# Kernel optimization log

Measured on AMD Instinct MI355X. Metric: run time of the kernel, lower is better.

## Reference

```python
import jax, jax.numpy as jnp
import numpy as np

SLOPE = 0.2  # LeakyReLU slope (DGCNN convention)

def _conv1x1(x, W, b):
    # x: [B, N, Cin], W: [Cout, Cin] -> [B, N, Cout] (Conv2d 1x1 == shared MLP)
    return jnp.einsum('bnc,oc->bno', x, W) + b

def _edgeconv(x, k, Wa, ba, Wb, bb):
    # DGCNN EdgeConv: kNN in feature space, edge MLP on (x_j - x_i, x_i), max-aggregate.
    # x: [B, N, C]
    sq = jnp.sum(x * x, axis=-1)                       # [B, N]
    inner = jnp.einsum('bnc,bmc->bnm', x, x)           # [B, N, N]
    dist = sq[:, :, None] - 2.0 * inner + sq[:, None, :]
    _, idx = jax.lax.top_k(-dist, k)                   # [B, N, k] (includes self)
    nb = jax.vmap(lambda xb, ib: xb[ib])(x, idx)       # [B, N, k, C] gather neighbors
    xi = jnp.broadcast_to(x[:, :, None, :], nb.shape)
    e = jnp.concatenate([nb - xi, xi], axis=-1)        # [B, N, k, 2C]
    h = jax.nn.leaky_relu(jnp.einsum('bnke,oe->bnko', e, Wa) + ba, SLOPE)
    h = jax.nn.leaky_relu(jnp.einsum('bnkc,oc->bnko', h, Wb) + bb, SLOPE)
    return jnp.max(h, axis=2)                          # [B, N, Cout]

def setup_inputs() -> dict:
    key = jax.random.key(0)
    ks = jax.random.split(key, 12)
    B, C, N = 2, 128, 8192
    r = 4
    out_dim = 3 * r  # 12
    def w(k, shape, fan_in):
        return (jax.random.normal(k, shape, jnp.float32) / np.sqrt(fan_in)).astype(jnp.float32)
    z = lambda n: jnp.zeros((n,), jnp.float32)
    return {
        'feature': jax.random.normal(ks[0], (B, C, N, 1), jnp.float32),
        # block 0: conv_bn_layer 128->32, EdgeConv(32->128, k=12)
        'Wc0': w(ks[1], (32, 128), 128), 'bc0': z(32),
        'We0a': w(ks[2], (128, 64), 64), 'be0a': z(128),
        'We0b': w(ks[3], (128, 128), 128), 'be0b': z(128),
        # block 1: conv_bn_layer 128->32, EdgeConv(32->128, k=4)
        'Wc1': w(ks[4], (32, 128), 128), 'bc1': z(32),
        'We1a': w(ks[5], (128, 64), 64), 'be1a': z(128),
        'We1b': w(ks[6], (128, 128), 128), 'be1b': z(128),
        # decoder: shared MLP [128 -> 6 -> 12], then Conv2d(12, 12, 1) with bias
        'Wd0': w(ks[7], (out_dim // 2, 128), 128), 'bd0': z(out_dim // 2),
        'Wd1': w(ks[8], (out_dim, out_dim // 2), out_dim // 2), 'bd1': z(out_dim),
        'Wd2': w(ks[9], (out_dim, out_dim), out_dim), 'bd2': z(out_dim),
    }

def reference(feature, Wc0, bc0, We0a, be0a, We0b, be0b,
              Wc1, bc1, We1a, be1a, We1b, be1b,
              Wd0, bd0, Wd1, bd1, Wd2, bd2):
    # feature: [B, C, N, 1] -> [B, N, C]
    x = jnp.swapaxes(jnp.squeeze(feature, -1), 1, 2)
    x = jax.nn.leaky_relu(_conv1x1(x, Wc0, bc0), SLOPE)   # 128 -> 32
    x = _edgeconv(x, 12, We0a, be0a, We0b, be0b)           # 32 -> 128, k=12
    x = jax.nn.leaky_relu(_conv1x1(x, Wc1, bc1), SLOPE)   # 128 -> 32
    x = _edgeconv(x, 4, We1a, be1a, We1b, be1b)            # 32 -> 128, k=4
    x = jax.nn.leaky_relu(_conv1x1(x, Wd0, bd0), SLOPE)   # 128 -> 6
    x = jax.nn.leaky_relu(_conv1x1(x, Wd1, bd1), SLOPE)   # 6 -> 12
    x = _conv1x1(x, Wd2, bd2)                              # final conv, no activation
    return x  # [B, N, 3*upsample_ratio] (matches squeeze(-1).permute(0,2,1))
```

## Files before the change

### kernel.cpp

```cpp
#include <hip/hip_runtime.h>

#define NPTS 8192
#define NB 2

typedef __attribute__((ext_vector_type(8))) short short8v;
typedef __attribute__((ext_vector_type(4))) float f32x4;

__device__ __forceinline__ float lrelu(float x) { return x > 0.f ? x : 0.2f * x; }
__device__ __forceinline__ float4 lrelu4(float4 a) {
    return make_float4(lrelu(a.x), lrelu(a.y), lrelu(a.z), lrelu(a.w));
}
__device__ __forceinline__ float4 fmax4(float4 a, float4 b) {
    return make_float4(fmaxf(a.x, b.x), fmaxf(a.y, b.y), fmaxf(a.z, b.z), fmaxf(a.w, b.w));
}
__device__ __forceinline__ float4 add4(float4 a, float4 b) {
    return make_float4(a.x + b.x, a.y + b.y, a.z + b.z, a.w + b.w);
}
__device__ __forceinline__ unsigned short f2bf(float f) {
    unsigned int u = __float_as_uint(f);
    return (unsigned short)((u + 0x7FFFu + ((u >> 16) & 1u)) >> 16);
}
__device__ __forceinline__ float bf2f(unsigned short h) {
    return __uint_as_float(((unsigned int)h) << 16);
}

__global__ void k_transpose_w(const float* __restrict__ Wb0, const float* __restrict__ Wb1,
                              float* __restrict__ out) {
    int t = blockIdx.x * 256 + threadIdx.x;
    if (t < 16384)      out[t] = Wb0[(t & 127) * 128 + (t >> 7)];
    else if (t < 32768) { int i = t - 16384; out[t] = Wb1[(i & 127) * 128 + (i >> 7)]; }
}

__device__ __forceinline__ void split3(float4 v, unsigned int* hp, unsigned int* mp,
                                       unsigned int* lp) {
    float c[4] = {v.x, v.y, v.z, v.w};
    unsigned short h[4], m[4], l[4];
    #pragma unroll
    for (int i = 0; i < 4; ++i) {
        h[i] = f2bf(c[i]);
        float r1 = c[i] - bf2f(h[i]);
        m[i] = f2bf(r1);
        float r2 = r1 - bf2f(m[i]);
        l[i] = f2bf(r2);
    }
    hp[0] = (unsigned int)h[0] | ((unsigned int)h[1] << 16);
    hp[1] = (unsigned int)h[2] | ((unsigned int)h[3] << 16);
    mp[0] = (unsigned int)m[0] | ((unsigned int)m[1] << 16);
    mp[1] = (unsigned int)m[2] | ((unsigned int)m[3] << 16);
    lp[0] = (unsigned int)l[0] | ((unsigned int)l[1] << 16);
    lp[1] = (unsigned int)l[2] | ((unsigned int)l[3] << 16);
}

__global__ void k_conv_in(const float* __restrict__ f, const float* __restrict__ W,
                          const float* __restrict__ bias, float* __restrict__ out,
                          float* __restrict__ sq, unsigned short* __restrict__ xh,
                          unsigned short* __restrict__ xm, unsigned short* __restrict__ xl) {
    int gid = blockIdx.x * blockDim.x + threadIdx.x;
    int b = gid >> 13, n = gid & (NPTS - 1);
    const float* fb = f + ((size_t)b << 20) + n;
    float acc[32];
    #pragma unroll
    for (int o = 0; o < 32; ++o) acc[o] = bias[o];
    #pragma unroll 4
    for (int c = 0; c < 128; ++c) {
        float xc = fb[(size_t)c * NPTS];
        #pragma unroll
        for (int o = 0; o < 32; ++o) acc[o] += xc * W[o * 128 + c];
    }
    float s = 0.f;
    float4* op = (float4*)(out + (size_t)gid * 32);
    unsigned int* hrow = (unsigned int*)(xh + (size_t)gid * 32);
    unsigned int* mrow = (unsigned int*)(xm + (size_t)gid * 32);
    unsigned int* lrow = (unsigned int*)(xl + (size_t)gid * 32);
    #pragma unroll
    for (int o4 = 0; o4 < 8; ++o4) {
        float4 v = make_float4(lrelu(acc[o4 * 4]), lrelu(acc[o4 * 4 + 1]),
                               lrelu(acc[o4 * 4 + 2]), lrelu(acc[o4 * 4 + 3]));
        s += v.x * v.x + v.y * v.y + v.z * v.z + v.w * v.w;
        op[o4] = v;
        unsigned int hp[2], mp[2], lp[2];
        split3(v, hp, mp, lp);
        *(uint2*)(hrow + o4 * 2) = make_uint2(hp[0], hp[1]);
        *(uint2*)(mrow + o4 * 2) = make_uint2(mp[0], mp[1]);
        *(uint2*)(lrow + o4 * 2) = make_uint2(lp[0], lp[1]);
    }
    sq[gid] = s;
}

__global__ __launch_bounds__(256, 2) void k_premix(const float* __restrict__ x,
                                                   const float* __restrict__ Wa,
                                                   const float* __restrict__ ba,
                                                   float* __restrict__ A,
                                                   float* __restrict__ Bm) {
    int tid = threadIdx.x;
    int q = tid >> 6;
    int p = blockIdx.x * 64 + (tid & 63);
    float4 xv[8];
    {
        const float4* xr = (const float4*)(x + (size_t)p * 32);
        #pragma unroll
        for (int u = 0; u < 8; ++u) xv[u] = xr[u];
    }
    const float* W0 = Wa + q * 32 * 64;
    float acc[32];
    #pragma unroll
    for (int o = 0; o < 32; ++o) acc[o] = 0.f;
    #pragma unroll 2
    for (int c4 = 0; c4 < 8; ++c4) {
        float4 v = xv[c4];
        #pragma unroll
        for (int o = 0; o < 32; ++o) {
            const float* w = W0 + o * 64 + c4 * 4;
            acc[o] += v.x * w[0] + v.y * w[1] + v.z * w[2] + v.w * w[3];
        }
    }
    {
        float4* op = (float4*)(A + (size_t)p * 128 + q * 32);
        #pragma unroll
        for (int o4 = 0; o4 < 8; ++o4)
            op[o4] = make_float4(acc[o4 * 4], acc[o4 * 4 + 1], acc[o4 * 4 + 2], acc[o4 * 4 + 3]);
    }
    #pragma unroll
    for (int o = 0; o < 32; ++o) acc[o] = ba[q * 32 + o];
    #pragma unroll 2
    for (int c4 = 0; c4 < 8; ++c4) {
        float4 v = xv[c4];
        #pragma unroll
        for (int o = 0; o < 32; ++o) {
            const float* w1 = W0 + o * 64 + c4 * 4;
            const float* w2 = w1 + 32;
            acc[o] += v.x * (w2[0] - w1[0]) + v.y * (w2[1] - w1[1]) +
                      v.z * (w2[2] - w1[2]) + v.w * (w2[3] - w1[3]);
        }
    }
    {
        float4* op = (float4*)(Bm + (size_t)p * 128 + q * 32);
        #pragma unroll
        for (int o4 = 0; o4 < 8; ++o4)
            op[o4] = make_float4(acc[o4 * 4], acc[o4 * 4 + 1], acc[o4 * 4 + 2], acc[o4 * 4 + 3]);
    }
}

template <int K, int JS, int C>
__global__ __launch_bounds__(128, 2) void k_knn_mfma(const unsigned short* __restrict__ xh,
                                                     const unsigned short* __restrict__ xm,
                                                     const unsigned short* __restrict__ xl,
                                                     const float* __restrict__ sqg,
                                                     float* __restrict__ cand_d,
                                                     int* __restrict__ cand_i) {
    constexpr int IT = 128;
    constexpr int JR = NPTS / JS;
    constexpr int NCH = JR / 16;
    constexpr int BPB = (NPTS / IT) * JS;
    constexpr int DS = 17;

    __shared__ float Dl[IT * DS];
    __shared__ float SQl[2][16];
    __shared__ float bufd[C * IT];
    __shared__ int   bufj[C * IT];

    int tid = threadIdx.x;
    int bid = blockIdx.x;
    int b = bid / BPB;
    int r0b = bid - b * BPB;
    int itile = r0b / JS;
    int jseg = r0b - itile * JS;

    const unsigned short* xhb = xh + ((size_t)b * NPTS) * 32;
    const unsigned short* xmb = xm + ((size_t)b * NPTS) * 32;
    const unsigned short* xlb = xl + ((size_t)b * NPTS) * 32;
    const float* sqb = sqg + (size_t)b * NPTS;

    int lane = tid & 63;
    int w = tid >> 6;
    int g = lane >> 4;
    int r15 = lane & 15;

    short8v ah[4], am[4], al[4];
    #pragma unroll
    for (int t = 0; t < 4; ++t) {
        size_t ii = (size_t)(itile * IT + w * 64 + t * 16 + r15);
        ah[t] = *(const short8v*)(xhb + ii * 32 + g * 8);
        am[t] = *(const short8v*)(xmb + ii * 32 + g * 8);
        al[t] = *(const short8v*)(xlb + ii * 32 + g * 8);
    }
    #pragma unroll
    for (int t = 0; t < 4; ++t) {
        asm volatile("" : "+v"(ah[t]));
        asm volatile("" : "+v"(am[t]));
        asm volatile("" : "+v"(al[t]));
    }

    float bd[K]; int bi[K];
    #pragma unroll
    for (int r = 0; r < K; ++r) { bd[r] = 1e30f; bi[r] = 0; }
    float thr = 1e30f;
    int cnt = 0;

    auto flush = [&]() {
        #pragma unroll
        for (int u = 0; u < C; ++u) {
            float dv = bufd[u * IT + tid];
            int jv = bufj[u * IT + tid];
            float dd = (u < cnt) ? dv : 1e30f;
            int ji = jv;
            #pragma unroll
            for (int r = 0; r < K; ++r) {
                bool c = dd < bd[r];
                float tf = bd[r]; int ti = bi[r];
                bd[r] = c ? dd : bd[r]; bi[r] = c ? ji : bi[r];
                dd = c ? tf : dd;       ji = c ? ti : ji;
            }
        }
        cnt = 0; thr = bd[K - 1];
    };

#define LOADB_(J, BH, BM, BL)                                                  \
    do {                                                                       \
        size_t ja_ = (size_t)(J) + r15;                                        \
        BH = *(const short8v*)(xhb + ja_ * 32 + g * 8);                        \
        BM = *(const short8v*)(xmb + ja_ * 32 + g * 8);                        \
        BL = *(const short8v*)(xlb + ja_ * 32 + g * 8);                        \
    } while (0)

#define SQSTAGE_(J0)                                                           \
    do {                                                                       \
        if (g == 0) SQl[w][r15] = sqb[(J0) + r15];                             \
    } while (0)

#define MFMA_(BH, BM, BL)                                                      \
    do {                                                                       \
        _Pragma("unroll")                                                      \
        for (int t = 0; t < 4; ++t) {                                          \
            f32x4 acc = {0.f, 0.f, 0.f, 0.f};                                  \
            acc = __builtin_amdgcn_mfma_f32_16x16x32_bf16(am[t], BM, acc, 0, 0, 0); \
            acc = __builtin_amdgcn_mfma_f32_16x16x32_bf16(ah[t], BL, acc, 0, 0, 0); \
            acc = __builtin_amdgcn_mfma_f32_16x16x32_bf16(al[t], BH, acc, 0, 0, 0); \
            acc = __builtin_amdgcn_mfma_f32_16x16x32_bf16(ah[t], BM, acc, 0, 0, 0); \
            acc = __builtin_amdgcn_mfma_f32_16x16x32_bf16(am[t], BH, acc, 0, 0, 0); \
            acc = __builtin_amdgcn_mfma_f32_16x16x32_bf16(ah[t], BH, acc, 0, 0, 0); \
            int il_ = w * 64 + t * 16 + g * 4;                                 \
            Dl[(il_ + 0) * DS + r15] = acc[0];                                 \
            Dl[(il_ + 1) * DS + r15] = acc[1];                                 \
            Dl[(il_ + 2) * DS + r15] = acc[2];                                 \
            Dl[(il_ + 3) * DS + r15] = acc[3];                                 \
        }                                                                      \
    } while (0)

#define SELECT_(J0)                                                            \
    do {                                                                       \
        _Pragma("unroll 1")                                                    \
        for (int jq = 0; jq < 16; jq += 4) {                                   \
            float v0 = Dl[tid * DS + jq + 0];                                  \
            float v1 = Dl[tid * DS + jq + 1];                                  \
            float v2 = Dl[tid * DS + jq + 2];                                  \
            float v3 = Dl[tid * DS + jq + 3];                                  \
            float s0 = SQl[w][jq + 0];                                         \
            float s1 = SQl[w][jq + 1];                                         \
            float s2 = SQl[w][jq + 2];                                         \
            float s3 = SQl[w][jq + 3];                                         \
            int j_ = (J0) + jq;                                                \
            float d0 = s0 - 2.f * v0;                                          \
            float d1 = s1 - 2.f * v1;                                          \
            float d2 = s2 - 2.f * v2;                                          \
            float d3 = s3 - 2.f * v3;                                          \
            if (d0 < thr) { bufd[cnt * IT + tid] = d0; bufj[cnt * IT + tid] = j_ + 0; cnt++; } \
            if (d1 < thr) { bufd[cnt * IT + tid] = d1; bufj[cnt * IT + tid] = j_ + 1; cnt++; } \
            if (d2 < thr) { bufd[cnt * IT + tid] = d2; bufj[cnt * IT + tid] = j_ + 2; cnt++; } \
            if (d3 < thr) { bufd[cnt * IT + tid] = d3; bufj[cnt * IT + tid] = j_ + 3; cnt++; } \
            if (__any(cnt >= C - 3)) flush();                                  \
        }                                                                      \
    } while (0)

    int jbase = jseg * JR;
    short8v bhA, bmA, blA, bhB, bmB, blB;
    LOADB_(jbase, bhA, bmA, blA);
    #pragma unroll 1
    for (int ch = 0; ch < NCH; ch += 2) {
        int j0 = jbase + ch * 16;
        int j1 = j0 + 16;
        SQSTAGE_(j0);
        LOADB_(j1, bhB, bmB, blB);
        MFMA_(bhA, bmA, blA);
        SELECT_(j0);
        SQSTAGE_(j1);
        int j2 = (ch + 2 < NCH) ? j1 + 16 : jbase;
        LOADB_(j2, bhA, bmA, blA);
        MFMA_(bhB, bmB, blB);
        SELECT_(j1);
    }
    flush();
#undef LOADB_
#undef SQSTAGE_
#undef MFMA_
#undef SELECT_
    size_t base = ((size_t)jseg * (NB * NPTS) + (size_t)(b * NPTS) + itile * IT + tid) * K;
    #pragma unroll
    for (int r = 0; r < K; ++r) { cand_d[base + r] = bd[r]; cand_i[base + r] = bi[r]; }
}

template <int K, int JS>
__global__ __launch_bounds__(128, 4) void k_knn_merge2(const float* __restrict__ cand_d,
                                                       const int* __restrict__ cand_i,
                                                       int* __restrict__ idx_out) {
    int p = blockIdx.x * 128 + threadIdx.x;
    float bd[K]; int bi[K];
    #pragma unroll
    for (int r = 0; r < K; ++r) { bd[r] = 1e30f; bi[r] = 0; }
    float thr = 1e30f;
    #pragma unroll 1
    for (int s = 0; s < JS; ++s) {
        size_t base = ((size_t)s * (NB * NPTS) + p) * K;
        #pragma unroll 1
        for (int r = 0; r < K; ++r) {
            float d = cand_d[base + r];
            if (!(d < thr)) break;
            int j = cand_i[base + r];
            float dd = d; int ji = j;
            #pragma unroll
            for (int q = 0; q < K; ++q) {
                bool c = dd < bd[q];
                float tf = bd[q]; int ti = bi[q];
                bd[q] = c ? dd : bd[q]; bi[q] = c ? ji : bi[q];
                dd = c ? tf : dd;       ji = c ? ti : ji;
            }
            thr = bd[K - 1];
        }
    }
    int* op = idx_out + (size_t)p * K;
    #pragma unroll
    for (int r = 0; r < K; ++r) op[r] = bi[r];
}

template <int K>
__global__ __launch_bounds__(256, 1)
void k_edgeconv4(const int* __restrict__ idx,
                 const float* __restrict__ A, const float* __restrict__ Bm,
                 const float* __restrict__ WbTg, const float* __restrict__ bb,
                 float* __restrict__ y) {
    constexpr int TE = (K == 12) ? 6 : 4;
    constexpr int EPI = 16 * TE;
    constexpr int PI = EPI / K;
    constexpr int ITERS = 64 / PI;
    constexpr int NT = 256;
    constexpr int HS = 132;

    __shared__ __align__(16) float WbT[128 * 128];
    __shared__ __align__(16) float bb_s[128];
    __shared__ __align__(16) float H1[EPI * HS];
    __shared__ __align__(16) float Pm[(K == 12) ? 16 * 128 : 4];

    int tid = threadIdx.x;
    {
        const float4* sb = (const float4*)WbTg;
        float4* db = (float4*)WbT;
        #pragma unroll
        for (int i = 0; i < 16; ++i) db[tid + i * NT] = sb[tid + i * NT];
        if (tid < 128) bb_s[tid] = bb[tid];
    }

    int b = blockIdx.x >> 7;
    int pbase = (blockIdx.x & 127) * 64;
    const int* idxb = idx + ((size_t)b * NPTS) * K;
    const float4* A4 = (const float4*)(A + ((size_t)b * NPTS) * 128);
    const float4* B4 = (const float4*)(Bm + ((size_t)b * NPTS) * 128);
    float* yb = y + ((size_t)b * NPTS) * 128;

    int og = tid & 15;
    int eg = tid >> 4;
    int ebase = eg * TE;

    for (int it = 0; it < ITERS; ++it) {
        int pt0 = pbase + it * PI;
        #pragma unroll
        for (int r = 0; r < (EPI * 32) / NT; ++r) {
            int u = tid + r * NT;
            int e = u >> 5, c4 = u & 31;
            int p = pt0 + e / K;
            int j = idxb[(size_t)p * K + (e % K)];
            float4 av = A4[(size_t)j * 32 + c4];
            float4 bv = B4[(size_t)p * 32 + c4];
            *(float4*)&H1[e * HS + 4 * c4] = lrelu4(add4(av, bv));
        }
        __syncthreads();
        float4 acc[TE][2];
        {
            float4 blo = *(const float4*)&bb_s[og * 8];
            float4 bhi = *(const float4*)&bb_s[og * 8 + 4];
            #pragma unroll
            for (int e = 0; e < TE; ++e) { acc[e][0] = blo; acc[e][1] = bhi; }
        }
        #pragma unroll 2
        for (int c4 = 0; c4 < 32; ++c4) {
            float4 hv[TE];
            #pragma unroll
            for (int e = 0; e < TE; ++e)
                hv[e] = *(const float4*)&H1[(ebase + e) * HS + 4 * c4];
            #pragma unroll
            for (int j = 0; j < 4; ++j) {
                const float* wr = &WbT[(4 * c4 + j) * 128 + og * 8];
                float4 wlo = *(const float4*)wr;
                float4 whi = *(const float4*)(wr + 4);
                #pragma unroll
                for (int e = 0; e < TE; ++e) {
                    float hc = (j == 0) ? hv[e].x : (j == 1) ? hv[e].y : (j == 2) ? hv[e].z : hv[e].w;
                    acc[e][0].x += hc * wlo.x; acc[e][0].y += hc * wlo.y;
                    acc[e][0].z += hc * wlo.z; acc[e][0].w += hc * wlo.w;
                    acc[e][1].x += hc * whi.x; acc[e][1].y += hc * whi.y;
                    acc[e][1].z += hc * whi.z; acc[e][1].w += hc * whi.w;
                }
            }
        }
        float4 mlo = lrelu4(acc[0][0]), mhi = lrelu4(acc[0][1]);
        #pragma unroll
        for (int e = 1; e < TE; ++e) {
            mlo = fmax4(mlo, lrelu4(acc[e][0]));
            mhi = fmax4(mhi, lrelu4(acc[e][1]));
        }
        if constexpr (K == 4) {
            float4* yp = (float4*)&yb[((size_t)(pt0 + eg)) * 128 + og * 8];
            yp[0] = mlo; yp[1] = mhi;
            __syncthreads();
        } else {
            *(float4*)&Pm[eg * 128 + og * 8] = mlo;
            *(float4*)&Pm[eg * 128 + og * 8 + 4] = mhi;
            __syncthreads();
            #pragma unroll
            for (int r = 0; r < 4; ++r) {
                int u = tid + r * NT;
                int p = u >> 7, o = u & 127;
                yb[((size_t)(pt0 + p)) * 128 + o] =
                    fmaxf(Pm[(2 * p) * 128 + o], Pm[(2 * p + 1) * 128 + o]);
            }
        }
    }
}

__global__ void k_conv_mid(const float* __restrict__ xin, const float* __restrict__ W,
                           const float* __restrict__ bias, float* __restrict__ out,
                           float* __restrict__ sq, unsigned short* __restrict__ xh,
                           unsigned short* __restrict__ xm, unsigned short* __restrict__ xl) {
    int gid = blockIdx.x * blockDim.x + threadIdx.x;
    const float4* row = (const float4*)(xin + (size_t)gid * 128);
    float acc[32];
    #pragma unroll
    for (int o = 0; o < 32; ++o) acc[o] = bias[o];
    #pragma unroll 2
    for (int c4 = 0; c4 < 32; ++c4) {
        float4 v = row[c4];
        #pragma unroll
        for (int o = 0; o < 32; ++o) {
            const float* w = W + o * 128 + c4 * 4;
            acc[o] += v.x * w[0] + v.y * w[1] + v.z * w[2] + v.w * w[3];
        }
    }
    float s = 0.f;
    float4* op = (float4*)(out + (size_t)gid * 32);
    unsigned int* hrow = (unsigned int*)(xh + (size_t)gid * 32);
    unsigned int* mrow = (unsigned int*)(xm + (size_t)gid * 32);
    unsigned int* lrow = (unsigned int*)(xl + (size_t)gid * 32);
    #pragma unroll
    for (int o4 = 0; o4 < 8; ++o4) {
        float4 v = make_float4(lrelu(acc[o4 * 4]), lrelu(acc[o4 * 4 + 1]),
                               lrelu(acc[o4 * 4 + 2]), lrelu(acc[o4 * 4 + 3]));
        s += v.x * v.x + v.y * v.y + v.z * v.z + v.w * v.w;
        op[o4] = v;
        unsigned int hp[2], mp[2], lp[2];
        split3(v, hp, mp, lp);
        *(uint2*)(hrow + o4 * 2) = make_uint2(hp[0], hp[1]);
        *(uint2*)(mrow + o4 * 2) = make_uint2(mp[0], mp[1]);
        *(uint2*)(lrow + o4 * 2) = make_uint2(lp[0], lp[1]);
    }
    sq[gid] = s;
}

__global__ void k_decoder(const float* __restrict__ xin,
                          const float* __restrict__ W0, const float* __restrict__ b0,
                          const float* __restrict__ W1, const float* __restrict__ b1,
                          const float* __restrict__ W2, const float* __restrict__ b2,
                          float* __restrict__ out) {
    int gid = blockIdx.x * blockDim.x + threadIdx.x;
    const float4* row = (const float4*)(xin + (size_t)gid * 128);
    float h0[6];
    #pragma unroll
    for (int o = 0; o < 6; ++o) h0[o] = b0[o];
    #pragma unroll 4
    for (int c4 = 0; c4 < 32; ++c4) {
        float4 v = row[c4];
        #pragma unroll
        for (int o = 0; o < 6; ++o) {
            const float* w = W0 + o * 128 + c4 * 4;
            h0[o] += v.x * w[0] + v.y * w[1] + v.z * w[2] + v.w * w[3];
        }
    }
    #pragma unroll
    for (int o = 0; o < 6; ++o) h0[o] = lrelu(h0[o]);
    float h1[12];
    #pragma unroll
    for (int o = 0; o < 12; ++o) {
        float a = b1[o];
        #pragma unroll
        for (int j = 0; j < 6; ++j) a += W1[o * 6 + j] * h0[j];
        h1[o] = lrelu(a);
    }
    float* op = out + (size_t)gid * 12;
    #pragma unroll
    for (int o = 0; o < 12; ++o) {
        float a = b2[o];
        #pragma unroll
        for (int j = 0; j < 12; ++j) a += W2[o * 12 + j] * h1[j];
        op[o] = a;
    }
}

extern "C" void kernel_launch(void* const* d_in, const int* in_sizes, int n_in,
                              void* d_out, int out_size, void* d_ws, size_t ws_size,
                              hipStream_t stream) {
    const float* feature = (const float*)d_in[0];
    const float* Wc0 = (const float*)d_in[1];
    const float* bc0 = (const float*)d_in[2];
    const float* We0a = (const float*)d_in[3];
    const float* be0a = (const float*)d_in[4];
    const float* We0b = (const float*)d_in[5];
    const float* be0b = (const float*)d_in[6];
    const float* Wc1 = (const float*)d_in[7];
    const float* bc1 = (const float*)d_in[8];
    const float* We1a = (const float*)d_in[9];
    const float* be1a = (const float*)d_in[10];
    const float* We1b = (const float*)d_in[11];
    const float* be1b = (const float*)d_in[12];
    const float* Wd0 = (const float*)d_in[13];
    const float* bd0 = (const float*)d_in[14];
    const float* Wd1 = (const float*)d_in[15];
    const float* bd1 = (const float*)d_in[16];
    const float* Wd2 = (const float*)d_in[17];
    const float* bd2 = (const float*)d_in[18];
    float* out = (float*)d_out;

    float* f = (float*)d_ws;
    float* x0   = f;
    float* x1   = f + 524288;
    int*   idx0 = (int*)(f + 1048576);
    int*   idx1 = (int*)(f + 1245184);
    float* wT   = f + 1310720;
    float* Zab  = f + 1343488;
    float* Abuf = Zab;
    float* Bbuf = Zab + 2097152;
    float* Y    = f + 5537792;
    float* sq0  = f + 7634944;
    float* sq1  = f + 7651328;
    unsigned short* xh0 = (unsigned short*)(f + 524288);
    unsigned short* xm0 = (unsigned short*)(f + 786432);
    unsigned short* xl0 = (unsigned short*)(f + 1048576);
    float* c0d  = f + 1343488;
    int*   c0i  = (int*)(f + 4489216);
    unsigned short* xh1 = (unsigned short*)Zab;
    unsigned short* xm1 = (unsigned short*)(Zab + 262144);
    unsigned short* xl1 = (unsigned short*)(Zab + 524288);
    float* c1d  = Zab + 786432;
    int*   c1i  = (int*)(Zab + 1835008);
    float* WbT0 = wT;
    float* WbT1 = wT + 16384;

    k_transpose_w<<<128, 256, 0, stream>>>(We0b, We1b, wT);
    k_conv_in<<<64, 256, 0, stream>>>(feature, Wc0, bc0, x0, sq0, xh0, xm0, xl0);
    k_knn_mfma<12, 16, 10><<<2048, 128, 0, stream>>>(xh0, xm0, xl0, sq0, c0d, c0i);
    k_knn_merge2<12, 16><<<128, 128, 0, stream>>>(c0d, c0i, idx0);
    k_premix<<<256, 256, 0, stream>>>(x0, We0a, be0a, Abuf, Bbuf);
    k_edgeconv4<12><<<256, 256, 0, stream>>>(idx0, Abuf, Bbuf, WbT0, be0b, Y);
    k_conv_mid<<<64, 256, 0, stream>>>(Y, Wc1, bc1, x1, sq1, xh1, xm1, xl1);
    k_knn_mfma<4, 16, 8><<<2048, 128, 0, stream>>>(xh1, xm1, xl1, sq1, c1d, c1i);
    k_knn_merge2<4, 16><<<128, 128, 0, stream>>>(c1d, c1i, idx1);
    k_premix<<<256, 256, 0, stream>>>(x1, We1a, be1a, Abuf, Bbuf);
    k_edgeconv4<4><<<256, 256, 0, stream>>>(idx1, Abuf, Bbuf, WbT1, be1b, Y);
    k_decoder<<<64, 256, 0, stream>>>(Y, Wd0, bd0, Wd1, bd1, Wd2, bd2, out);
}
```

Before: 634.1 us.

## Fold -2 scale and squared-norm bias into MFMA, pack kNN candidates

Pre-scales the A-side bf16 split operands by -2 using exponent-bit arithmetic and seeds the MFMA accumulator with each column's squared norm. The MFMA output is then the distance directly, which removes the shared-memory SQ staging and the per-element FMA in selection. Candidate distance and index are packed into a single 64-bit LDS entry. The flush now loops only to the wave-max candidate count instead of the full buffer. The exponent trick assumes no bf16 value is zero, denormal or near overflow, and a zero component would be corrupted, so correctness is a risk.

Result: no change. 623.6 us (-1.6%).

```diff
diff --git a/kernel.cpp b/kernel.cpp
--- a/kernel.cpp
+++ b/kernel.cpp
@@ -22,6 +22,14 @@
 }
 __device__ __forceinline__ float bf2f(unsigned short h) {
     return __uint_as_float(((unsigned int)h) << 16);
+}
+__device__ __forceinline__ short8v scale_m2(short8v v) {
+    uint4 u = *(uint4*)&v;
+    u.x = (u.x + 0x00800080u) ^ 0x80008000u;
+    u.y = (u.y + 0x00800080u) ^ 0x80008000u;
+    u.z = (u.z + 0x00800080u) ^ 0x80008000u;
+    u.w = (u.w + 0x00800080u) ^ 0x80008000u;
+    return *(short8v*)&u;
 }
 
 __global__ void k_transpose_w(const float* __restrict__ Wb0, const float* __restrict__ Wb1,
@@ -155,9 +163,7 @@
     constexpr int DS = 17;
 
     __shared__ float Dl[IT * DS];
-    __shared__ float SQl[2][16];
-    __shared__ float bufd[C * IT];
-    __shared__ int   bufj[C * IT];
+    __shared__ unsigned long long bufe[C * IT];
 
     int tid = threadIdx.x;
     int bid = blockIdx.x;
@@ -180,9 +186,9 @@
     #pragma unroll
     for (int t = 0; t < 4; ++t) {
         size_t ii = (size_t)(itile * IT + w * 64 + t * 16 + r15);
-        ah[t] = *(const short8v*)(xhb + ii * 32 + g * 8);
-        am[t] = *(const short8v*)(xmb + ii * 32 + g * 8);
-        al[t] = *(const short8v*)(xlb + ii * 32 + g * 8);
+        ah[t] = scale_m2(*(const short8v*)(xhb + ii * 32 + g * 8));
+        am[t] = scale_m2(*(const short8v*)(xmb + ii * 32 + g * 8));
+        al[t] = scale_m2(*(const short8v*)(xlb + ii * 32 + g * 8));
     }
     #pragma unroll
     for (int t = 0; t < 4; ++t) {
@@ -198,12 +204,18 @@
     int cnt = 0;
 
     auto flush = [&]() {
-        #pragma unroll
-        for (int u = 0; u < C; ++u) {
-            float dv = bufd[u * IT + tid];
-            int jv = bufj[u * IT + tid];
-            float dd = (u < cnt) ? dv : 1e30f;
-            int ji = jv;
+        int mc = cnt;
+        #pragma unroll
+        for (int off = 1; off < 64; off <<= 1) {
+            int o = __shfl_xor(mc, off);
+            mc = mc > o ? mc : o;
+        }
+        #pragma unroll 1
+        for (int u = 0; u < mc; ++u) {
+            unsigned long long e = bufe[u * IT + tid];
+            bool valid = u < cnt;
+            float dd = valid ? __uint_as_float((unsigned int)(e >> 32)) : 1e30f;
+            int ji = (int)(unsigned int)e;
             #pragma unroll
             for (int r = 0; r < K; ++r) {
                 bool c = dd < bd[r];
@@ -215,24 +227,20 @@
         cnt = 0; thr = bd[K - 1];
     };
 
-#define LOADB_(J, BH, BM, BL)                                                  \
+#define LOADBS_(J, BH, BM, BL, SV)                                             \
     do {                                                                       \
         size_t ja_ = (size_t)(J) + r15;                                        \
         BH = *(const short8v*)(xhb + ja_ * 32 + g * 8);                        \
         BM = *(const short8v*)(xmb + ja_ * 32 + g * 8);                        \
         BL = *(const short8v*)(xlb + ja_ * 32 + g * 8);                        \
+        SV = sqb[(size_t)(J) + r15];                                           \
     } while (0)
 
-#define SQSTAGE_(J0)                                                           \
-    do {                                                                       \
-        if (g == 0) SQl[w][r15] = sqb[(J0) + r15];                             \
-    } while (0)
-
-#define MFMA_(BH, BM, BL)                                                      \
+#define MFMA_(BH, BM, BL, SV)                                                  \
     do {                                                                       \
         _Pragma("unroll")                                                      \
         for (int t = 0; t < 4; ++t) {                                          \
-            f32x4 acc = {0.f, 0.f, 0.f, 0.f};                                  \
+            f32x4 acc = {SV, SV, SV, SV};                                      \
             acc = __builtin_amdgcn_mfma_f32_16x16x32_bf16(am[t], BM, acc, 0, 0, 0); \
             acc = __builtin_amdgcn_mfma_f32_16x16x32_bf16(ah[t], BL, acc, 0, 0, 0); \
             acc = __builtin_amdgcn_mfma_f32_16x16x32_bf16(al[t], BH, acc, 0, 0, 0); \
@@ -247,52 +255,45 @@
         }                                                                      \
     } while (0)
 
+#define PACK_(D, J) ((((unsigned long long)__float_as_uint(D)) << 32) | (unsigned int)(J))
+
 #define SELECT_(J0)                                                            \
     do {                                                                       \
         _Pragma("unroll 1")                                                    \
         for (int jq = 0; jq < 16; jq += 4) {                                   \
-            float v0 = Dl[tid * DS + jq + 0];                                  \
-            float v1 = Dl[tid * DS + jq + 1];                                  \
-            float v2 = Dl[tid * DS + jq + 2];                                  \
-            float v3 = Dl[tid * DS + jq + 3];                                  \
-            float s0 = SQl[w][jq + 0];                                         \
-            float s1 = SQl[w][jq + 1];                                         \
-            float s2 = SQl[w][jq + 2];                                         \
-            float s3 = SQl[w][jq + 3];                                         \
+            float d0 = Dl[tid * DS + jq + 0];                                  \
+            float d1 = Dl[tid * DS + jq + 1];                                  \
+            float d2 = Dl[tid * DS + jq + 2];                                  \
+            float d3 = Dl[tid * DS + jq + 3];                                  \
             int j_ = (J0) + jq;                                                \
-            float d0 = s0 - 2.f * v0;                                          \
-            float d1 = s1 - 2.f * v1;                                          \
-            float d2 = s2 - 2.f * v2;                                          \
-            float d3 = s3 - 2.f * v3;                                          \
-            if (d0 < thr) { bufd[cnt * IT + tid] = d0; bufj[cnt * IT + tid] = j_ + 0; cnt++; } \
-            if (d1 < thr) { bufd[cnt * IT + tid] = d1; bufj[cnt * IT + tid] = j_ + 1; cnt++; } \
-            if (d2 < thr) { bufd[cnt * IT + tid] = d2; bufj[cnt * IT + tid] = j_ + 2; cnt++; } \
-            if (d3 < thr) { bufd[cnt * IT + tid] = d3; bufj[cnt * IT + tid] = j_ + 3; cnt++; } \
+            if (d0 < thr) { bufe[cnt * IT + tid] = PACK_(d0, j_ + 0); cnt++; } \
+            if (d1 < thr) { bufe[cnt * IT + tid] = PACK_(d1, j_ + 1); cnt++; } \
+            if (d2 < thr) { bufe[cnt * IT + tid] = PACK_(d2, j_ + 2); cnt++; } \
+            if (d3 < thr) { bufe[cnt * IT + tid] = PACK_(d3, j_ + 3); cnt++; } \
             if (__any(cnt >= C - 3)) flush();                                  \
         }                                                                      \
     } while (0)
 
     int jbase = jseg * JR;
     short8v bhA, bmA, blA, bhB, bmB, blB;
-    LOADB_(jbase, bhA, bmA, blA);
+    float svA, svB;
+    LOADBS_(jbase, bhA, bmA, blA, svA);
     #pragma unroll 1
     for (int ch = 0; ch < NCH; ch += 2) {
         int j0 = jbase + ch * 16;
         int j1 = j0 + 16;
-        SQSTAGE_(j0);
-        LOADB_(j1, bhB, bmB, blB);
-        MFMA_(bhA, bmA, blA);
+        LOADBS_(j1, bhB, bmB, blB, svB);
+        MFMA_(bhA, bmA, blA, svA);
         SELECT_(j0);
-        SQSTAGE_(j1);
         int j2 = (ch + 2 < NCH) ? j1 + 16 : jbase;
-        LOADB_(j2, bhA, bmA, blA);
-        MFMA_(bhB, bmB, blB);
+        LOADBS_(j2, bhA, bmA, blA, svA);
+        MFMA_(bhB, bmB, blB, svB);
         SELECT_(j1);
     }
     flush();
-#undef LOADB_
-#undef SQSTAGE_
+#undef LOADBS_
 #undef MFMA_
+#undef PACK_
 #undef SELECT_
     size_t base = ((size_t)jseg * (NB * NPTS) + (size_t)(b * NPTS) + itile * IT + tid) * K;
     #pragma unroll
```
